# Kernel optimization log

Measured on AMD Instinct MI355X. Metric: run time of the kernel, lower is better.

The kernel has to match this reference:

```python
import jax, jax.numpy as jnp
import numpy as np


def setup_inputs() -> dict:
    key = jax.random.key(0)
    k1, k2, k3, k4 = jax.random.split(key, 4)
    B, S, D = 8, 2048, 1024
    x = jax.random.normal(k1, (B, S, D), dtype=jnp.float32)
    scale = 1.0 / np.sqrt(D)  # glorot-ish magnitude
    Wq = jax.random.normal(k2, (D, D), dtype=jnp.float32) * scale
    Wk = jax.random.normal(k3, (D, D), dtype=jnp.float32) * scale
    Wv = jax.random.normal(k4, (D, D), dtype=jnp.float32) * scale
    return {"x": x, "Wq": Wq, "Wk": Wk, "Wv": Wv}


def reference(x, Wq, Wk, Wv):
    # q,k,v: [B,S,D]
    q = jnp.einsum("bsd,de->bse", x, Wq)
    k = jnp.einsum("bsd,de->bse", x, Wk)
    v = jnp.einsum("bsd,de->bse", x, Wv)
    d = k.shape[-1]
    # scores: [B,S,S], scaled by sqrt(d)
    scores = jnp.einsum("bqd,bkd->bqk", q, k) / jnp.sqrt(jnp.asarray(d, x.dtype))
    attn = jax.nn.softmax(scores, axis=-1)
    out = jnp.einsum("bqk,bkd->bqd", attn, v)
    return out
```

## Files before the change

### kernel.cpp

```cpp
#include <hip/hip_runtime.h>
#include <hip/hip_bf16.h>

typedef __bf16 bf16x8 __attribute__((ext_vector_type(8)));
typedef float  f32x4  __attribute__((ext_vector_type(4)));

static __device__ __forceinline__ unsigned short f2bf(float f) {
  unsigned int u = __float_as_uint(f);
  u += 0x7FFFu + ((u >> 16) & 1u);
  return (unsigned short)(u >> 16);
}

static __device__ __forceinline__ void gl_lds16(const void* g, void* l) {
  __builtin_amdgcn_global_load_lds(
      (const __attribute__((address_space(1))) void*)g,
      (__attribute__((address_space(3))) void*)l,
      16, 0, 0);
}

__global__ __launch_bounds__(256) void cast_f32_bf16(
    const float* __restrict__ in, unsigned short* __restrict__ out, int n) {
  int i = (blockIdx.x * 256 + threadIdx.x) * 4;
  const int stride = gridDim.x * 256 * 4;
  for (; i < n; i += stride) {
    float4 f = *(const float4*)(in + i);
    ushort4 o;
    o.x = f2bf(f.x); o.y = f2bf(f.y); o.z = f2bf(f.z); o.w = f2bf(f.w);
    *(ushort4*)(out + i) = o;
  }
}

__global__ __launch_bounds__(256) void transpose_cast_w(
    const float* __restrict__ w, unsigned short* __restrict__ wt) {
  __shared__ float tile[16][17];
  const int tx = threadIdx.x & 15, ty = threadIdx.x >> 4;
  const int bx = blockIdx.x * 16, by = blockIdx.y * 16;
  tile[ty][tx] = w[(size_t)(by + ty) * 1024 + bx + tx];
  __syncthreads();
  wt[(size_t)(bx + ty) * 1024 + by + tx] = f2bf(tile[tx][ty]);
}

template <int MODE>
__global__ __launch_bounds__(256, 2) void gemm_bt(
    const unsigned short* __restrict__ A, int lda, size_t astride,
    const unsigned short* __restrict__ B, int ldb, size_t bstride,
    int K, void* __restrict__ Cv, int ldc, size_t cstride,
    float* __restrict__ aux) {
  __shared__ __align__(16) unsigned char lds[32768];
  const unsigned d2 = blockIdx.x + gridDim.x * blockIdx.y;
  const unsigned ty = d2 % gridDim.y;
  const unsigned tx = d2 / gridDim.y;
  const int bn0 = tx * 128;
  const int bm0 = ty * 128;
  A += (size_t)blockIdx.z * astride;
  B += (size_t)blockIdx.z * bstride;

  const int tid = threadIdx.x;
  const int wid = tid >> 6, lane = tid & 63;
  const int wr = wid >> 1, wc = wid & 1;
  const int l15 = lane & 15, kq = lane >> 4;

  const int sr = tid >> 2;
  const int ssub = (tid & 3) * 8;
  size_t aoff[4], boff[4];
#pragma unroll
  for (int j = 0; j < 4; ++j) {
    const int r = (j & 1) * 64 + sr;
    const int kko = (j >> 1) * 32;
    aoff[j] = (size_t)(bm0 + r) * lda + kko + ssub;
    boff[j] = (size_t)(bn0 + r) * ldb + kko + ssub;
  }
  unsigned char* dstA = lds + wid * 1024;
  unsigned char* dstB = lds + 16384 + wid * 1024;

  f32x4 acc[4][4] = {};
  const int nkt = K >> 6;
  for (int kt = 0; kt < nkt; ++kt) {
    const int kc = kt << 6;
#pragma unroll
    for (int j = 0; j < 4; ++j) {
      gl_lds16(A + aoff[j] + kc, dstA + j * 4096);
      gl_lds16(B + boff[j] + kc, dstB + j * 4096);
    }
    __syncthreads();

#pragma unroll
    for (int kk = 0; kk < 2; ++kk) {
      bf16x8 af[4], bg[4];
#pragma unroll
      for (int mi = 0; mi < 4; ++mi)
        af[mi] = *(const bf16x8*)(lds + kk * 8192 + (wr * 64 + mi * 16 + l15) * 64 + kq * 16);
#pragma unroll
      for (int ni = 0; ni < 4; ++ni)
        bg[ni] = *(const bf16x8*)(lds + 16384 + kk * 8192 + (wc * 64 + ni * 16 + l15) * 64 + kq * 16);
#pragma unroll
      for (int mi = 0; mi < 4; ++mi)
#pragma unroll
        for (int ni = 0; ni < 4; ++ni)
          acc[mi][ni] = __builtin_amdgcn_mfma_f32_16x16x32_bf16(af[mi], bg[ni], acc[mi][ni], 0, 0, 0);
    }
    __syncthreads();
  }

  if constexpr (MODE == 3) {
#pragma unroll
    for (int mi = 0; mi < 4; ++mi)
#pragma unroll
      for (int ni = 0; ni < 4; ++ni)
#pragma unroll
        for (int r = 0; r < 4; ++r) {
          const int row = bm0 + wr * 64 + mi * 16 + kq * 4 + r;
          const int col = bn0 + wc * 64 + ni * 16 + l15;
          const float v = acc[mi][ni][r];
          unsigned short* q = (unsigned short*)Cv;
          if (col < 1024) {
            q[(size_t)row * 1024 + col] = f2bf(v);
          } else if (col < 2048) {
            q[16777216u + (size_t)row * 1024 + (col - 1024)] = f2bf(v);
          } else {
            const int b = row >> 11, s = row & 2047;
            q[33554432u + ((size_t)(b * 1024 + (col - 2048))) * 2048 + s] = f2bf(v);
          }
        }
  } else if constexpr (MODE == 4) {
    __shared__ float redsm[128][2];
    unsigned short* pp = (unsigned short*)Cv + (size_t)blockIdx.z * cstride;
    float rs[4][4];
#pragma unroll
    for (int mi = 0; mi < 4; ++mi)
#pragma unroll
      for (int r = 0; r < 4; ++r) rs[mi][r] = 0.f;
#pragma unroll
    for (int mi = 0; mi < 4; ++mi)
#pragma unroll
      for (int ni = 0; ni < 4; ++ni)
#pragma unroll
        for (int r = 0; r < 4; ++r) {
          const float e = exp2f(acc[mi][ni][r] * 0.045084220027780106f);
          rs[mi][r] += e;
          const int row = bm0 + wr * 64 + mi * 16 + kq * 4 + r;
          const int col = bn0 + wc * 64 + ni * 16 + l15;
          pp[(size_t)row * ldc + col] = f2bf(e);
        }
#pragma unroll
    for (int mi = 0; mi < 4; ++mi)
#pragma unroll
      for (int r = 0; r < 4; ++r) {
        float s = rs[mi][r];
        s += __shfl_xor(s, 1); s += __shfl_xor(s, 2);
        s += __shfl_xor(s, 4); s += __shfl_xor(s, 8);
        rs[mi][r] = s;
      }
    if (l15 == 0) {
#pragma unroll
      for (int mi = 0; mi < 4; ++mi)
#pragma unroll
        for (int r = 0; r < 4; ++r)
          redsm[wr * 64 + mi * 16 + kq * 4 + r][wc] = rs[mi][r];
    }
    __syncthreads();
    if (tid < 128)
      aux[((size_t)blockIdx.z * 16 + tx) * 2048 + bm0 + tid] =
          redsm[tid][0] + redsm[tid][1];
  } else {
    const float* inv = aux + (size_t)blockIdx.z * 2048;
    float* op = (float*)Cv + (size_t)blockIdx.z * cstride;
#pragma unroll
    for (int mi = 0; mi < 4; ++mi)
#pragma unroll
      for (int r = 0; r < 4; ++r) {
        const int row = bm0 + wr * 64 + mi * 16 + kq * 4 + r;
        const float iv = inv[row];
#pragma unroll
        for (int ni = 0; ni < 4; ++ni) {
          const int col = bn0 + wc * 64 + ni * 16 + l15;
          op[(size_t)row * ldc + col] = acc[mi][ni][r] * iv;
        }
      }
  }
}

__global__ __launch_bounds__(256) void combine_inv(
    const float* __restrict__ part, float* __restrict__ inv, int n) {
  const int i = blockIdx.x * 256 + threadIdx.x;
  if (i >= n) return;
  const int z = i >> 11, row = i & 2047;
  const float* p = part + ((size_t)z * 16) * 2048 + row;
  float s = 0.f;
#pragma unroll
  for (int j = 0; j < 16; ++j) s += p[j * 2048];
  inv[i] = 1.0f / s;
}

extern "C" void kernel_launch(void* const* d_in, const int* in_sizes, int n_in,
                              void* d_out, int out_size, void* d_ws, size_t ws_size,
                              hipStream_t stream) {
  const float* x  = (const float*)d_in[0];
  const float* Wq = (const float*)d_in[1];
  const float* Wk = (const float*)d_in[2];
  const float* Wv = (const float*)d_in[3];
  float* out = (float*)d_out;
  char* ws = (char*)d_ws;

  unsigned short* xb     = (unsigned short*)ws;
  unsigned short* wt_all = (unsigned short*)(ws + 33554432);
  unsigned short* qb     = (unsigned short*)(ws + 39845888);
  unsigned short* kb     = qb + 16777216;
  unsigned short* vt     = kb + 16777216;
  const size_t off_scores = 140509184ull;

  const size_t per_b = 8388608ull + 131072ull + 8192ull;
  int G; char *pPc, *partc, *invc;
  const size_t avail = ws_size > off_scores ? ws_size - off_scores : 0;
  G = (int)(avail / per_b); if (G > 8) G = 8;
  if (G >= 1) {
    pPc   = ws + off_scores;
    partc = pPc + (size_t)G * 8388608ull;
    invc  = partc + (size_t)G * 131072ull;
  } else {
    G = 2;
    pPc   = ws;
    partc = ws + 2 * 8388608ull;
    invc  = partc + 2 * 131072ull;
  }

  cast_f32_bf16<<<2048, 256, 0, stream>>>(x, xb, 16384 * 1024);
  transpose_cast_w<<<dim3(64, 64), 256, 0, stream>>>(Wq, wt_all);
  transpose_cast_w<<<dim3(64, 64), 256, 0, stream>>>(Wk, wt_all + 1048576);
  transpose_cast_w<<<dim3(64, 64), 256, 0, stream>>>(Wv, wt_all + 2097152);

  gemm_bt<3><<<dim3(24, 128), 256, 0, stream>>>(xb, 1024, 0, wt_all, 1024, 0,
                                                1024, qb, 0, 0, nullptr);

  for (int b0 = 0; b0 < 8; b0 += G) {
    const int g = (8 - b0) < G ? (8 - b0) : G;
    const size_t so = (size_t)b0 * 2097152;
    gemm_bt<4><<<dim3(16, 16, g), 256, 0, stream>>>(
        qb + so, 1024, 2097152, kb + so, 1024, 2097152, 1024,
        (unsigned short*)pPc, 2048, 4194304, (float*)partc);
    combine_inv<<<(g * 2048 + 255) / 256, 256, 0, stream>>>(
        (const float*)partc, (float*)invc, g * 2048);
    gemm_bt<5><<<dim3(8, 16, g), 256, 0, stream>>>(
        (const unsigned short*)pPc, 2048, 4194304,
        vt + so, 2048, 2097152, 2048,
        out + so, 1024, 2097152, (float*)invc);
  }
}
```

Measured before the change: 346.2 us.

## Use 256x256 tile QKV GEMM, merge weight transposes, fold row-sum combine

The fused QKV projection moves to a new 512-thread kernel with 256x256 output tiles and a 32-wide K step, which raises reuse per LDS load. The three weight transpose launches become one 3D-grid launch. The separate combine_inv kernel is dropped, and the PV GEMM now sums the partial row sums itself and keeps the inverse in shared memory. This cuts launch count and intermediate traffic, at the cost of higher register pressure (32 accumulators per thread) and more barriers per K in the big GEMM.

```diff
diff --git a/kernel.cpp b/kernel.cpp
--- a/kernel.cpp
+++ b/kernel.cpp
@@ -29,14 +29,88 @@
   }
 }
 
-__global__ __launch_bounds__(256) void transpose_cast_w(
-    const float* __restrict__ w, unsigned short* __restrict__ wt) {
+__global__ __launch_bounds__(256) void transpose_cast_w3(
+    const float* __restrict__ w0, const float* __restrict__ w1,
+    const float* __restrict__ w2, unsigned short* __restrict__ wt) {
   __shared__ float tile[16][17];
+  const float* w = blockIdx.z == 0 ? w0 : (blockIdx.z == 1 ? w1 : w2);
+  unsigned short* o = wt + (size_t)blockIdx.z * 1048576;
   const int tx = threadIdx.x & 15, ty = threadIdx.x >> 4;
   const int bx = blockIdx.x * 16, by = blockIdx.y * 16;
   tile[ty][tx] = w[(size_t)(by + ty) * 1024 + bx + tx];
   __syncthreads();
-  wt[(size_t)(bx + ty) * 1024 + by + tx] = f2bf(tile[tx][ty]);
+  o[(size_t)(bx + ty) * 1024 + by + tx] = f2bf(tile[tx][ty]);
+}
+
+__global__ __launch_bounds__(512, 2) void gemm256s(
+    const unsigned short* __restrict__ A, int lda,
+    const unsigned short* __restrict__ B, int ldb,
+    int K, void* __restrict__ Cv) {
+  __shared__ __align__(16) unsigned char lds[32768];
+  const unsigned d2 = blockIdx.x + gridDim.x * blockIdx.y;
+  const unsigned ty = d2 % gridDim.y;
+  const unsigned tx = d2 / gridDim.y;
+  const int bm0 = ty * 256;
+  const int bn0 = tx * 256;
+
+  const int tid = threadIdx.x;
+  const int wid = tid >> 6, lane = tid & 63;
+  const int wr = wid >> 2, wc = wid & 3;
+  const int l15 = lane & 15, kq = lane >> 4;
+
+  const size_t aoff0 = (size_t)(bm0 + (tid >> 2)) * lda + (tid & 3) * 8;
+  const size_t aoff1 = aoff0 + (size_t)128 * lda;
+  const size_t boff0 = (size_t)(bn0 + (tid >> 2)) * ldb + (tid & 3) * 8;
+  const size_t boff1 = boff0 + (size_t)128 * ldb;
+  unsigned char* dA0 = lds + wid * 1024;
+  unsigned char* dA1 = lds + 8192 + wid * 1024;
+  unsigned char* dB0 = lds + 16384 + wid * 1024;
+  unsigned char* dB1 = lds + 24576 + wid * 1024;
+
+  f32x4 acc[8][4] = {};
+  const int nkt = K >> 5;
+  for (int kt = 0; kt < nkt; ++kt) {
+    const int kc = kt << 5;
+    gl_lds16(A + aoff0 + kc, dA0);
+    gl_lds16(A + aoff1 + kc, dA1);
+    gl_lds16(B + boff0 + kc, dB0);
+    gl_lds16(B + boff1 + kc, dB1);
+    __syncthreads();
+
+    bf16x8 af[8], bg[4];
+#pragma unroll
+    for (int mi = 0; mi < 8; ++mi)
+      af[mi] = *(const bf16x8*)(lds + (wr * 128 + mi * 16 + l15) * 64 + kq * 16);
+#pragma unroll
+    for (int ni = 0; ni < 4; ++ni)
+      bg[ni] = *(const bf16x8*)(lds + 16384 + (wc * 64 + ni * 16 + l15) * 64 + kq * 16);
+#pragma unroll
+    for (int mi = 0; mi < 8; ++mi)
+#pragma unroll
+      for (int ni = 0; ni < 4; ++ni)
+        acc[mi][ni] = __builtin_amdgcn_mfma_f32_16x16x32_bf16(af[mi], bg[ni], acc[mi][ni], 0, 0, 0);
+    __syncthreads();
+  }
+
+#pragma unroll
+  for (int mi = 0; mi < 8; ++mi)
+#pragma unroll
+    for (int ni = 0; ni < 4; ++ni)
+#pragma unroll
+      for (int r = 0; r < 4; ++r) {
+        const int row = bm0 + wr * 128 + mi * 16 + kq * 4 + r;
+        const int col = bn0 + wc * 64 + ni * 16 + l15;
+        const float v = acc[mi][ni][r];
+        unsigned short* q = (unsigned short*)Cv;
+        if (col < 1024) {
+          q[(size_t)row * 1024 + col] = f2bf(v);
+        } else if (col < 2048) {
+          q[16777216u + (size_t)row * 1024 + (col - 1024)] = f2bf(v);
+        } else {
+          const int b = row >> 11, s = row & 2047;
+          q[33554432u + ((size_t)(b * 1024 + (col - 2048))) * 2048 + s] = f2bf(v);
+        }
+      }
 }
 
 template <int MODE>
@@ -46,6 +120,7 @@
     int K, void* __restrict__ Cv, int ldc, size_t cstride,
     float* __restrict__ aux) {
   __shared__ __align__(16) unsigned char lds[32768];
+  __shared__ float smInv[128];
   const unsigned d2 = blockIdx.x + gridDim.x * blockIdx.y;
   const unsigned ty = d2 % gridDim.y;
   const unsigned tx = d2 / gridDim.y;
@@ -59,6 +134,16 @@
   const int wr = wid >> 1, wc = wid & 1;
   const int l15 = lane & 15, kq = lane >> 4;
 
+  if constexpr (MODE == 5) {
+    if (tid < 128) {
+      const float* p = aux + (size_t)blockIdx.z * 32768 + bm0 + tid;
+      float s = 0.f;
+#pragma unroll
+      for (int j = 0; j < 16; ++j) s += p[j * 2048];
+      smInv[tid] = 1.0f / s;
+    }
+  }
+
   const int sr = tid >> 2;
   const int ssub = (tid & 3) * 8;
   size_t aoff[4], boff[4];
@@ -101,27 +186,7 @@
     __syncthreads();
   }
 
-  if constexpr (MODE == 3) {
-#pragma unroll
-    for (int mi = 0; mi < 4; ++mi)
-#pragma unroll
-      for (int ni = 0; ni < 4; ++ni)
-#pragma unroll
-        for (int r = 0; r < 4; ++r) {
-          const int row = bm0 + wr * 64 + mi * 16 + kq * 4 + r;
-          const int col = bn0 + wc * 64 + ni * 16 + l15;
-          const float v = acc[mi][ni][r];
-          unsigned short* q = (unsigned short*)Cv;
-          if (col < 1024) {
-            q[(size_t)row * 1024 + col] = f2bf(v);
-          } else if (col < 2048) {
-            q[16777216u + (size_t)row * 1024 + (col - 1024)] = f2bf(v);
-          } else {
-            const int b = row >> 11, s = row & 2047;
-            q[33554432u + ((size_t)(b * 1024 + (col - 2048))) * 2048 + s] = f2bf(v);
-          }
-        }
-  } else if constexpr (MODE == 4) {
+  if constexpr (MODE == 4) {
     __shared__ float redsm[128][2];
     unsigned short* pp = (unsigned short*)Cv + (size_t)blockIdx.z * cstride;
     float rs[4][4];
@@ -162,14 +227,13 @@
       aux[((size_t)blockIdx.z * 16 + tx) * 2048 + bm0 + tid] =
           redsm[tid][0] + redsm[tid][1];
   } else {
-    const float* inv = aux + (size_t)blockIdx.z * 2048;
     float* op = (float*)Cv + (size_t)blockIdx.z * cstride;
 #pragma unroll
     for (int mi = 0; mi < 4; ++mi)
 #pragma unroll
       for (int r = 0; r < 4; ++r) {
         const int row = bm0 + wr * 64 + mi * 16 + kq * 4 + r;
-        const float iv = inv[row];
+        const float iv = smInv[wr * 64 + mi * 16 + kq * 4 + r];
 #pragma unroll
         for (int ni = 0; ni < 4; ++ni) {
           const int col = bn0 + wc * 64 + ni * 16 + l15;
@@ -177,18 +241,6 @@
         }
       }
   }
-}
-
-__global__ __launch_bounds__(256) void combine_inv(
-    const float* __restrict__ part, float* __restrict__ inv, int n) {
-  const int i = blockIdx.x * 256 + threadIdx.x;
-  if (i >= n) return;
-  const int z = i >> 11, row = i & 2047;
-  const float* p = part + ((size_t)z * 16) * 2048 + row;
-  float s = 0.f;
-#pragma unroll
-  for (int j = 0; j < 16; ++j) s += p[j * 2048];
-  inv[i] = 1.0f / s;
 }
 
 extern "C" void kernel_launch(void* const* d_in, const int* in_sizes, int n_in,
@@ -208,28 +260,23 @@
   unsigned short* vt     = kb + 16777216;
   const size_t off_scores = 140509184ull;
 
-  const size_t per_b = 8388608ull + 131072ull + 8192ull;
-  int G; char *pPc, *partc, *invc;
+  const size_t per_b = 8388608ull + 131072ull;
+  int G; char *pPc, *partc;
   const size_t avail = ws_size > off_scores ? ws_size - off_scores : 0;
   G = (int)(avail / per_b); if (G > 8) G = 8;
   if (G >= 1) {
     pPc   = ws + off_scores;
     partc = pPc + (size_t)G * 8388608ull;
-    invc  = partc + (size_t)G * 131072ull;
   } else {
     G = 2;
     pPc   = ws;
     partc = ws + 2 * 8388608ull;
-    invc  = partc + 2 * 131072ull;
   }
 
   cast_f32_bf16<<<2048, 256, 0, stream>>>(x, xb, 16384 * 1024);
-  transpose_cast_w<<<dim3(64, 64), 256, 0, stream>>>(Wq, wt_all);
-  transpose_cast_w<<<dim3(64, 64), 256, 0, stream>>>(Wk, wt_all + 1048576);
-  transpose_cast_w<<<dim3(64, 64), 256, 0, stream>>>(Wv, wt_all + 2097152);
-
-  gemm_bt<3><<<dim3(24, 128), 256, 0, stream>>>(xb, 1024, 0, wt_all, 1024, 0,
-                                                1024, qb, 0, 0, nullptr);
+  transpose_cast_w3<<<dim3(64, 64, 3), 256, 0, stream>>>(Wq, Wk, Wv, wt_all);
+
+  gemm256s<<<dim3(12, 64), 512, 0, stream>>>(xb, 1024, wt_all, 1024, 1024, qb);
 
   for (int b0 = 0; b0 < 8; b0 += G) {
     const int g = (8 - b0) < G ? (8 - b0) : G;
@@ -237,11 +284,9 @@
     gemm_bt<4><<<dim3(16, 16, g), 256, 0, stream>>>(
         qb + so, 1024, 2097152, kb + so, 1024, 2097152, 1024,
         (unsigned short*)pPc, 2048, 4194304, (float*)partc);
-    combine_inv<<<(g * 2048 + 255) / 256, 256, 0, stream>>>(
-        (const float*)partc, (float*)invc, g * 2048);
     gemm_bt<5><<<dim3(8, 16, g), 256, 0, stream>>>(
         (const unsigned short*)pPc, 2048, 4194304,
         vt + so, 2048, 2097152, 2048,
-        out + so, 1024, 2097152, (float*)invc);
-  }
-}
+        out + so, 1024, 2097152, (float*)partc);
+  }
+}
```

Result: slower. 362.5 us (+4.7%).
